# Kernel optimization log

Measured on AMD Instinct MI355X. Metric: run time of the kernel, lower is better.

The kernel has to match this reference:

```python
import jax, jax.numpy as jnp
import numpy as np

HEADS = 8
DK = 64   # key_size (defaults to size_per_head)
DV = 64   # size_per_head
RATE = 4
OUT = HEADS * DV  # 512


def extract_seq_patches(x, kernel, rate):
    # x: [b, L, d] -> [b, L, kernel, d]; strided local window gather
    b, L, d = x.shape
    k_size = kernel + (rate - 1) * (kernel - 1)
    p_right = (k_size - 1) // 2
    p_left = k_size - 1 - p_right
    xp = jnp.pad(x, ((0, 0), (p_left, p_right), (0, 0)))
    patches = [xp[:, i:i + L] for i in range(0, k_size, rate)]  # kernel slices
    return jnp.stack(patches, axis=2)


def setup_inputs() -> dict:
    key = jax.random.key(0)
    k1, k2, k3, k4 = jax.random.split(key, 4)
    s = 1.0 / np.sqrt(OUT)
    x = jax.random.normal(k1, (2, 4096, OUT), dtype=jnp.float32)
    Wq = jax.random.normal(k2, (OUT, HEADS * DK), dtype=jnp.float32) * s
    Wk = jax.random.normal(k3, (OUT, HEADS * DK), dtype=jnp.float32) * s
    Wv = jax.random.normal(k4, (OUT, HEADS * DV), dtype=jnp.float32) * s
    return {"x": x, "Wq": Wq, "Wk": Wk, "Wv": Wv}


def reference(x, Wq, Wk, Wv):
    b, L, d = x.shape
    pad = RATE - L % RATE  # torch code always pads (pad=RATE when L % RATE == 0)
    xpad = jnp.pad(x, ((0, 0), (0, pad), (0, 0)))
    nL = L + pad
    n = nL // RATE
    kernel = 2 * RATE - 1  # 1 + 2*neighbors

    qw = xpad @ Wq
    kw = xpad @ Wk
    vw = xpad @ Wv

    kwp = extract_seq_patches(kw, kernel, RATE)  # [b, nL, K, H*dk]
    vwp = extract_seq_patches(vw, kernel, RATE)  # [b, nL, K, H*dv]

    # [b, h, r, n, d]
    qw = qw.reshape(b, n, RATE, HEADS, DK).transpose(0, 3, 2, 1, 4)
    kw = kw.reshape(b, n, RATE, HEADS, DK).transpose(0, 3, 2, 1, 4)
    vw = vw.reshape(b, n, RATE, HEADS, DV).transpose(0, 3, 2, 1, 4)
    # [b, h, r, n, K, d]
    kwp = kwp.reshape(b, n, RATE, kernel, HEADS, DK).transpose(0, 4, 2, 1, 3, 5)
    vwp = vwp.reshape(b, n, RATE, kernel, HEADS, DV).transpose(0, 4, 2, 1, 3, 5)

    scale = 1.0 / np.sqrt(DK)
    a = jnp.einsum('bhrnd,bhrmd->bhrnm', qw, kw) * scale    # strided scores [b,h,r,n,n]
    ap = jnp.einsum('bhrnd,bhrnkd->bhrnk', qw, kwp) * scale  # local scores  [b,h,r,n,K]

    A = jax.nn.softmax(jnp.concatenate([a, ap], axis=-1), axis=-1)
    a, ap = A[..., :n], A[..., n:]

    o = jnp.einsum('bhrnm,bhrmd->bhrnd', a, vw) + jnp.einsum('bhrnk,bhrnkd->bhrnd', ap, vwp)
    o = o.transpose(0, 3, 2, 1, 4).reshape(b, nL, HEADS * DV)
    return o[:, :L]
```

## Files before the change

### kernel.cpp

```cpp
#include <hip/hip_runtime.h>
#include <hip/hip_bf16.h>


#define BATCH 2
#define LSEQ  4096
#define DMODEL 512
#define NH    8
#define DHEAD 64
#define NPAD  1088
#define QSCALE 0.18033688011112042f

typedef __bf16 bf16x8 __attribute__((ext_vector_type(8)));
typedef __attribute__((ext_vector_type(4))) float f32x4;
typedef __attribute__((ext_vector_type(16))) float f32x16;
typedef unsigned short u16;
typedef unsigned int u32;
typedef __attribute__((ext_vector_type(8))) u16 u16x8;
typedef __attribute__((ext_vector_type(4))) u16 u16x4;
typedef __attribute__((ext_vector_type(4))) u32 u32x4;

__device__ __forceinline__ u16 f2bf(float f) {
    u32 u = __float_as_uint(f);
    u += 0x7fffu + ((u >> 16) & 1u);
    return (u16)(u >> 16);
}

__device__ __forceinline__ u32 cvtpk(float lo, float hi) {
    u32 d;
    asm("v_cvt_pk_bf16_f32 %0, %1, %2" : "=v"(d) : "v"(lo), "v"(hi));
    return d;
}

__device__ __forceinline__ void gload16(const u16* g, u16* l) {
    __builtin_amdgcn_global_load_lds(
        (const __attribute__((address_space(1))) u32*)(const void*)g,
        (__attribute__((address_space(3))) u32*)(void*)l, 16, 0, 0);
}

__device__ __forceinline__ f32x16 zero16() {
    f32x16 v;
    #pragma unroll
    for (int i = 0; i < 16; ++i) v[i] = 0.f;
    return v;
}

__global__ __launch_bounds__(256) void prep_kernel(
    const float* __restrict__ x,
    const float* __restrict__ Wq, const float* __restrict__ Wk, const float* __restrict__ Wv,
    u16* __restrict__ xb, u16* __restrict__ Wt)
{
    const int bid = blockIdx.x, tid = threadIdx.x;
    if (bid < 2048) {
        const size_t i0 = (size_t)bid * 2048 + (size_t)tid * 8;
        float4 a = *(const float4*)(x + i0);
        float4 b = *(const float4*)(x + i0 + 4);
        u16x8 o = { f2bf(a.x), f2bf(a.y), f2bf(a.z), f2bf(a.w),
                    f2bf(b.x), f2bf(b.y), f2bf(b.z), f2bf(b.w) };
        *(u16x8*)(xb + i0) = o;
    } else {
        const int wb  = bid - 2048;
        const int mat = wb >> 6;
        const int t   = wb & 63;
        const int k0  = (t >> 3) * 64, c0 = (t & 7) * 64;
        const float* W = (mat == 0) ? Wq : (mat == 1) ? Wk : Wv;
        __shared__ u16 Ws[64][72];
        #pragma unroll
        for (int i = 0; i < 4; ++i) {
            const int chunk = i * 256 + tid;
            const int kr = chunk >> 4, c4 = (chunk & 15) * 4;
            float4 v = *(const float4*)(W + (size_t)(k0 + kr) * DMODEL + c0 + c4);
            u16x4 q = { f2bf(v.x), f2bf(v.y), f2bf(v.z), f2bf(v.w) };
            *(u16x4*)&Ws[kr][c4] = q;
        }
        __syncthreads();
        const int cc = tid >> 2, kq = (tid & 3) * 16;
        alignas(16) u16 tmp[16];
        #pragma unroll
        for (int kk = 0; kk < 16; ++kk) tmp[kk] = Ws[kq + kk][cc];
        u16* dst = Wt + (size_t)(mat * 512 + c0 + cc) * DMODEL + k0 + kq;
        *(u16x8*)dst       = *(const u16x8*)&tmp[0];
        *(u16x8*)(dst + 8) = *(const u16x8*)&tmp[8];
    }
}

__global__ __launch_bounds__(256) void gemm_kernel(
    const u16* __restrict__ xb, const u16* __restrict__ Wt,
    u16* __restrict__ Qb, u16* __restrict__ Kb, u16* __restrict__ Vb)
{
    const int bid = blockIdx.x;
    const int xcd = bid & 7;
    const int j   = bid >> 3;
    const int mt  = xcd * 8 + (j / 12);
    const int nt  = j % 12;
    const int m0 = mt * 128;
    const int n0 = nt * 128;
    const int tid = threadIdx.x;
    const int w = tid >> 6, l = tid & 63, lr = l & 15, lh = l >> 4;
    const int wr = w >> 1, wc = w & 1;

    __shared__ u16 smem[16896];
    u16* As = smem;
    u16* Bs = smem + 8192;

    f32x4 acc[4][4];
    const f32x4 fzero = {0.f, 0.f, 0.f, 0.f};
    #pragma unroll
    for (int mi = 0; mi < 4; ++mi)
        #pragma unroll
        for (int nj = 0; nj < 4; ++nj) acc[mi][nj] = fzero;

    for (int kt = 0; kt < 8; ++kt) {
        const int k0 = kt * 64;
        #pragma unroll
        for (int i = 0; i < 4; ++i) {
            const int cid = i * 256 + tid;
            const int row = cid >> 3, ch = cid & 7;
            const int sch = ch ^ (row & 7);
            u16* dstA = As + (i * 256 + w * 64) * 8;
            u16* dstB = Bs + (i * 256 + w * 64) * 8;
            gload16(xb + (size_t)(m0 + row) * DMODEL + k0 + sch * 8, dstA);
            gload16(Wt + (size_t)(n0 + row) * DMODEL + k0 + sch * 8, dstB);
        }
        __syncthreads();

        #pragma unroll
        for (int kk = 0; kk < 2; ++kk) {
            const int cs = (kk * 4 + lh) ^ (lr & 7);
            bf16x8 af[4], bfr[4];
            #pragma unroll
            for (int mi = 0; mi < 4; ++mi)
                af[mi] = *(const bf16x8*)(As + (wr * 64 + mi * 16 + lr) * 64 + cs * 8);
            #pragma unroll
            for (int nj = 0; nj < 4; ++nj)
                bfr[nj] = *(const bf16x8*)(Bs + (wc * 64 + nj * 16 + lr) * 64 + cs * 8);
            #pragma unroll
            for (int mi = 0; mi < 4; ++mi)
                #pragma unroll
                for (int nj = 0; nj < 4; ++nj)
                    acc[mi][nj] = __builtin_amdgcn_mfma_f32_16x16x32_bf16(af[mi], bfr[nj], acc[mi][nj], 0, 0, 0);
        }
        __syncthreads();
    }

    const int mat = nt >> 2;
    const int hp  = nt & 3;
    if (mat < 2) {
        u16* Ob = (mat == 0) ? Qb : Kb;
        const float osc = (mat == 0) ? QSCALE : 1.0f;
        #pragma unroll
        for (int mi = 0; mi < 4; ++mi) {
            const int gmb = m0 + wr * 64 + mi * 16 + lh * 4;
            const int b = gmb >> 12;
            #pragma unroll
            for (int rr = 0; rr < 4; ++rr) {
                const int t = (gmb + rr) & 4095;
                const int n = t >> 2, r = t & 3;
                #pragma unroll
                for (int nj = 0; nj < 4; ++nj) {
                    const int c  = wc * 64 + nj * 16 + lr;
                    const int h  = hp * 2 + (c >> 6);
                    const int dk = c & 63;
                    const size_t g = ((size_t)(b * NH + h)) * 4 + r;
                    Ob[(g * NPAD + n) * DHEAD + dk] = f2bf(acc[mi][nj][rr] * osc);
                }
            }
        }
    } else {
        #pragma unroll
        for (int mi = 0; mi < 4; ++mi) {
            const int nrel = wr * 16 + mi * 4 + lh;
            #pragma unroll
            for (int nj = 0; nj < 4; ++nj) {
                const int c = wc * 64 + nj * 16 + lr;
                #pragma unroll
                for (int rr = 0; rr < 4; ++rr)
                    smem[c * 132 + rr * 32 + nrel] = f2bf(acc[mi][nj][rr]);
            }
        }
        __syncthreads();
        const int b  = m0 >> 12;
        const int nb = (m0 & 4095) >> 2;
        #pragma unroll
        for (int e = 0; e < 2; ++e) {
            const int chunk = e * 256 + tid;
            const int c = chunk & 127, r = chunk >> 7;
            const int h  = hp * 2 + (c >> 6);
            const int dv = c & 63;
            const size_t g = ((size_t)(b * NH + h)) * 4 + r;
            u16* dst = Vb + (g * DHEAD + dv) * NPAD + nb;
            const u16* src = smem + c * 132 + r * 32;
            alignas(16) u16 tmp[32];
            #pragma unroll
            for (int q8 = 0; q8 < 8; ++q8)
                *(u16x4*)&tmp[q8 * 4] = *(const u16x4*)(src + q8 * 4);
            #pragma unroll
            for (int q16 = 0; q16 < 4; ++q16)
                *(u16x8*)(dst + q16 * 8) = *(const u16x8*)&tmp[q16 * 8];
        }
    }
}

__global__ __launch_bounds__(256) void attn_kernel(
    const u16* __restrict__ Qb, const u16* __restrict__ Kb, const u16* __restrict__ Vb,
    float* __restrict__ out)
{
    const int g  = blockIdx.x;
    const int b  = g >> 5;
    const int h  = (g >> 2) & 7;
    const int r  = g & 3;
    const int q0 = blockIdx.y * 128;
    const int tid = threadIdx.x;
    const int w  = tid >> 6;
    const int l  = tid & 63;
    const int lr = l & 31;
    const int hi = l >> 5;

    const u16* Qg  = Qb + (size_t)g * NPAD * DHEAD;
    const u16* Kg  = Kb + (size_t)g * NPAD * DHEAD;
    const u16* Vtg = Vb + (size_t)g * DHEAD * NPAD;

    __shared__ u16 KV[2][2][4096];

    const int srow = tid >> 3;
    const int ssch = (tid & 7) ^ (srow & 7);
    const u16* ksrc0 = Kg  + (size_t)srow * DHEAD + ssch * 8;
    const u16* vsrc0 = Vtg + (size_t)srow * NPAD  + ssch * 8;

    bf16x8 qa[4];
    {
        const u16* qrow = Qg + (size_t)(q0 + w * 32 + lr) * DHEAD + hi * 8;
        qa[0] = *(const bf16x8*)(qrow);
        qa[1] = *(const bf16x8*)(qrow + 16);
        qa[2] = *(const bf16x8*)(qrow + 32);
        qa[3] = *(const bf16x8*)(qrow + 48);
    }

    f32x16 o0 = zero16(), o1 = zero16();
    float Lown = 0.f;
    const int qw0 = q0 + w * 32;
    const int qg  = qw0 + lr;

    gload16(ksrc0,              &KV[0][0][w * 512]);
    gload16(ksrc0 + 32 * DHEAD, &KV[0][0][2048 + w * 512]);
    gload16(vsrc0,              &KV[0][1][w * 512]);
    gload16(vsrc0 + 32 * NPAD,  &KV[0][1][2048 + w * 512]);

    for (int mt = 0; mt < 16; ++mt) {
        const int cur = mt & 1;
        if (mt < 15) {
            const size_t ko = (size_t)(mt + 1) * 64 * DHEAD;
            const int    vo = (mt + 1) * 64;
            gload16(ksrc0 + ko,              &KV[cur ^ 1][0][w * 512]);
            gload16(ksrc0 + ko + 32 * DHEAD, &KV[cur ^ 1][0][2048 + w * 512]);
            gload16(vsrc0 + vo,              &KV[cur ^ 1][1][w * 512]);
            gload16(vsrc0 + vo + 32 * NPAD,  &KV[cur ^ 1][1][2048 + w * 512]);
            asm volatile("s_waitcnt vmcnt(4)" ::: "memory");
        } else {
            asm volatile("s_waitcnt vmcnt(0)" ::: "memory");
        }
        __builtin_amdgcn_s_barrier();

        const u16* Kbuf = KV[cur][0];
        const u16* Vbuf = KV[cur][1];

        f32x16 sA = zero16(), sB = zero16();
        __builtin_amdgcn_s_setprio(1);
        #pragma unroll
        for (int c = 0; c < 4; ++c) {
            const int slot = (c * 2 + hi) ^ (lr & 7);
            bf16x8 kbA = *(const bf16x8*)(Kbuf + (lr * 8 + slot) * 8);
            bf16x8 kbB = *(const bf16x8*)(Kbuf + ((32 + lr) * 8 + slot) * 8);
            sA = __builtin_amdgcn_mfma_f32_32x32x16_bf16(kbA, qa[c], sA, 0, 0, 0);
            sB = __builtin_amdgcn_mfma_f32_32x32x16_bf16(kbB, qa[c], sB, 0, 0, 0);
        }
        __builtin_amdgcn_s_setprio(0);

        const int m0 = mt * 64;
        const bool special = (m0 + 66 >= qw0) && (m0 <= qw0 + 34);
        if (!special) {
            #pragma unroll
            for (int reg = 0; reg < 16; ++reg) {
                sA[reg] = __builtin_amdgcn_exp2f(sA[reg]);
                sB[reg] = __builtin_amdgcn_exp2f(sB[reg]);
                Lown += sA[reg] + sB[reg];
            }
        } else {
            #pragma unroll
            for (int reg = 0; reg < 16; ++reg) {
                const int krel = (reg & 3) + 8 * (reg >> 2) + 4 * hi;
                {
                    const int dd = m0 + krel - qg;
                    float v = sA[reg];
                    if (dd >= -3 && dd <= 3) v += 1.0f;
                    sA[reg] = __builtin_amdgcn_exp2f(v);
                }
                {
                    const int dd = m0 + 32 + krel - qg;
                    float v = sB[reg];
                    if (dd >= -3 && dd <= 3) v += 1.0f;
                    sB[reg] = __builtin_amdgcn_exp2f(v);
                }
                Lown += sA[reg] + sB[reg];
            }
        }

        u32 pkA[8], pkB[8];
        #pragma unroll
        for (int r2 = 0; r2 < 8; ++r2) {
            pkA[r2] = cvtpk(sA[2 * r2], sA[2 * r2 + 1]);
            pkB[r2] = cvtpk(sB[2 * r2], sB[2 * r2 + 1]);
        }

        __builtin_amdgcn_s_setprio(1);
        #pragma unroll
        for (int c = 0; c < 4; ++c) {
            const int c1 = c & 1;
            u32 p0, p1, p2, p3;
            if (c < 2) { p0 = pkA[4*c1]; p1 = pkA[4*c1+1]; p2 = pkA[4*c1+2]; p3 = pkA[4*c1+3]; }
            else       { p0 = pkB[4*c1]; p1 = pkB[4*c1+1]; p2 = pkB[4*c1+2]; p3 = pkB[4*c1+3]; }
            const u32 own0  = hi ? p2 : p0;
            const u32 own1  = hi ? p3 : p1;
            const u32 send0 = hi ? p0 : p2;
            const u32 send1 = hi ? p1 : p3;
            const u32 recv0 = (u32)__shfl_xor((int)send0, 32);
            const u32 recv1 = (u32)__shfl_xor((int)send1, 32);
            u32x4 paw;
            paw.x = hi ? recv0 : own0;
            paw.y = hi ? recv1 : own1;
            paw.z = hi ? own0  : recv0;
            paw.w = hi ? own1  : recv1;
            const bf16x8 pa = __builtin_bit_cast(bf16x8, paw);

            const int slot = (c * 2 + hi) ^ (lr & 7);
            bf16x8 vb0 = *(const bf16x8*)(Vbuf + (lr * 8 + slot) * 8);
            bf16x8 vb1 = *(const bf16x8*)(Vbuf + ((32 + lr) * 8 + slot) * 8);
            o0 = __builtin_amdgcn_mfma_f32_32x32x16_bf16(pa, vb0, o0, 0, 0, 0);
            o1 = __builtin_amdgcn_mfma_f32_32x32x16_bf16(pa, vb1, o1, 0, 0, 0);
        }
        __builtin_amdgcn_s_setprio(0);
        __syncthreads();
    }

    const float Ltot = Lown + __shfl_xor(Lown, 32);
    const int coob = (qg < 3 ? 3 - qg : 0) + (qg > 1021 ? qg - 1021 : 0);
    const float inv = 1.0f / (Ltot + (float)(coob + 1 + (qg >= 1021 ? 1 : 0)));

    float iv[16];
    #pragma unroll
    for (int reg = 0; reg < 16; ++reg)
        iv[reg] = __shfl(inv, (reg & 3) + 8 * (reg >> 2) + 4 * hi);

    #pragma unroll
    for (int reg = 0; reg < 16; ++reg) {
        const int qrel = (reg & 3) + 8 * (reg >> 2) + 4 * hi;
        const int t = (q0 + w * 32 + qrel) * 4 + r;
        float* orow = out + ((size_t)b * LSEQ + t) * DMODEL + h * DHEAD;
        orow[lr]      = o0[reg] * iv[reg];
        orow[32 + lr] = o1[reg] * iv[reg];
    }
}

extern "C" void kernel_launch(void* const* d_in, const int* in_sizes, int n_in,
                              void* d_out, int out_size, void* d_ws, size_t ws_size,
                              hipStream_t stream) {
    const float* x  = (const float*)d_in[0];
    const float* Wq = (const float*)d_in[1];
    const float* Wk = (const float*)d_in[2];
    const float* Wv = (const float*)d_in[3];
    float* out = (float*)d_out;

    const size_t SZ = (size_t)BATCH * NH * 4 * NPAD * DHEAD;
    u16* Qb = (u16*)d_ws;
    u16* Kb = Qb + SZ;
    u16* Vb = Kb + SZ;

    u16* xb = (u16*)d_out;
    u16* Wt = xb + (size_t)8192 * 512;

    prep_kernel<<<2240, 256, 0, stream>>>(x, Wq, Wk, Wv, xb, Wt);

    gemm_kernel<<<768, 256, 0, stream>>>(xb, Wt, Qb, Kb, Vb);

    dim3 ga(64, 8);
    attn_kernel<<<ga, 256, 0, stream>>>(Qb, Kb, Vb, out);
}
```

Before: 67.68 us.

## Split attention key range across two wave groups with shared-memory reduction

Doubles the attention block to 512 threads, so two groups of four waves each process half of the key tiles (8 iterations instead of 16) for the same 128 queries. Partial output accumulators and row sums from the second group are reduced through shared memory before normalization and the store. The aim is to halve the serial loop length per block and raise waves per CU, since the grid has only 512 blocks. The cost is doubled LDS per block, an extra reduction phase with barriers, and tighter register limits from the new launch bounds.

```diff
diff --git a/kernel.cpp b/kernel.cpp
--- a/kernel.cpp
+++ b/kernel.cpp
@@ -200,7 +200,7 @@
     }
 }
 
-__global__ __launch_bounds__(256) void attn_kernel(
+__global__ __launch_bounds__(512, 4) void attn_kernel(
     const u16* __restrict__ Qb, const u16* __restrict__ Kb, const u16* __restrict__ Vb,
     float* __restrict__ out)
 {
@@ -211,6 +211,8 @@
     const int q0 = blockIdx.y * 128;
     const int tid = threadIdx.x;
     const int w  = tid >> 6;
+    const int wq = w & 3;
+    const int kh = w >> 2;
     const int l  = tid & 63;
     const int lr = l & 31;
     const int hi = l >> 5;
@@ -219,7 +221,9 @@
     const u16* Kg  = Kb + (size_t)g * NPAD * DHEAD;
     const u16* Vtg = Vb + (size_t)g * DHEAD * NPAD;
 
-    __shared__ u16 KV[2][2][4096];
+    __shared__ __align__(16) u16 KV[2][2][2][4096];
+    float* red  = (float*)&KV[0][0][0][0];
+    float* redL = red + 4 * 64 * 33;
 
     const int srow = tid >> 3;
     const int ssch = (tid & 7) ^ (srow & 7);
@@ -228,7 +232,7 @@
 
     bf16x8 qa[4];
     {
-        const u16* qrow = Qg + (size_t)(q0 + w * 32 + lr) * DHEAD + hi * 8;
+        const u16* qrow = Qg + (size_t)(q0 + wq * 32 + lr) * DHEAD + hi * 8;
         qa[0] = *(const bf16x8*)(qrow);
         qa[1] = *(const bf16x8*)(qrow + 16);
         qa[2] = *(const bf16x8*)(qrow + 32);
@@ -237,31 +241,31 @@
 
     f32x16 o0 = zero16(), o1 = zero16();
     float Lown = 0.f;
-    const int qw0 = q0 + w * 32;
+    const int qw0 = q0 + wq * 32;
     const int qg  = qw0 + lr;
 
-    gload16(ksrc0,              &KV[0][0][w * 512]);
-    gload16(ksrc0 + 32 * DHEAD, &KV[0][0][2048 + w * 512]);
-    gload16(vsrc0,              &KV[0][1][w * 512]);
-    gload16(vsrc0 + 32 * NPAD,  &KV[0][1][2048 + w * 512]);
-
-    for (int mt = 0; mt < 16; ++mt) {
+    gload16(ksrc0,                      &KV[0][0][0][w * 512]);
+    gload16(ksrc0 + (size_t)512 * DHEAD, &KV[0][1][0][w * 512]);
+    gload16(vsrc0,                      &KV[0][0][1][w * 512]);
+    gload16(vsrc0 + 512,                &KV[0][1][1][w * 512]);
+
+    for (int mt = 0; mt < 8; ++mt) {
         const int cur = mt & 1;
-        if (mt < 15) {
+        if (mt < 7) {
             const size_t ko = (size_t)(mt + 1) * 64 * DHEAD;
             const int    vo = (mt + 1) * 64;
-            gload16(ksrc0 + ko,              &KV[cur ^ 1][0][w * 512]);
-            gload16(ksrc0 + ko + 32 * DHEAD, &KV[cur ^ 1][0][2048 + w * 512]);
-            gload16(vsrc0 + vo,              &KV[cur ^ 1][1][w * 512]);
-            gload16(vsrc0 + vo + 32 * NPAD,  &KV[cur ^ 1][1][2048 + w * 512]);
+            gload16(ksrc0 + ko,                       &KV[cur ^ 1][0][0][w * 512]);
+            gload16(ksrc0 + ko + (size_t)512 * DHEAD, &KV[cur ^ 1][1][0][w * 512]);
+            gload16(vsrc0 + vo,                       &KV[cur ^ 1][0][1][w * 512]);
+            gload16(vsrc0 + vo + 512,                 &KV[cur ^ 1][1][1][w * 512]);
             asm volatile("s_waitcnt vmcnt(4)" ::: "memory");
         } else {
             asm volatile("s_waitcnt vmcnt(0)" ::: "memory");
         }
         __builtin_amdgcn_s_barrier();
 
-        const u16* Kbuf = KV[cur][0];
-        const u16* Vbuf = KV[cur][1];
+        const u16* Kbuf = &KV[cur][kh][0][0];
+        const u16* Vbuf = &KV[cur][kh][1][0];
 
         f32x16 sA = zero16(), sB = zero16();
         __builtin_amdgcn_s_setprio(1);
@@ -275,8 +279,8 @@
         }
         __builtin_amdgcn_s_setprio(0);
 
-        const int m0 = mt * 64;
-        const bool special = (m0 + 66 >= qw0) && (m0 <= qw0 + 34);
+        const int mabs = kh * 512 + mt * 64;
+        const bool special = (mabs + 66 >= qw0) && (mabs <= qw0 + 34);
         if (!special) {
             #pragma unroll
             for (int reg = 0; reg < 16; ++reg) {
@@ -289,13 +293,13 @@
             for (int reg = 0; reg < 16; ++reg) {
                 const int krel = (reg & 3) + 8 * (reg >> 2) + 4 * hi;
                 {
-                    const int dd = m0 + krel - qg;
+                    const int dd = mabs + krel - qg;
                     float v = sA[reg];
                     if (dd >= -3 && dd <= 3) v += 1.0f;
                     sA[reg] = __builtin_amdgcn_exp2f(v);
                 }
                 {
-                    const int dd = m0 + 32 + krel - qg;
+                    const int dd = mabs + 32 + krel - qg;
                     float v = sB[reg];
                     if (dd >= -3 && dd <= 3) v += 1.0f;
                     sB[reg] = __builtin_amdgcn_exp2f(v);
@@ -338,25 +342,46 @@
             o1 = __builtin_amdgcn_mfma_f32_32x32x16_bf16(pa, vb1, o1, 0, 0, 0);
         }
         __builtin_amdgcn_s_setprio(0);
-        __syncthreads();
-    }
-
-    const float Ltot = Lown + __shfl_xor(Lown, 32);
-    const int coob = (qg < 3 ? 3 - qg : 0) + (qg > 1021 ? qg - 1021 : 0);
-    const float inv = 1.0f / (Ltot + (float)(coob + 1 + (qg >= 1021 ? 1 : 0)));
-
-    float iv[16];
-    #pragma unroll
-    for (int reg = 0; reg < 16; ++reg)
-        iv[reg] = __shfl(inv, (reg & 3) + 8 * (reg >> 2) + 4 * hi);
-
-    #pragma unroll
-    for (int reg = 0; reg < 16; ++reg) {
-        const int qrel = (reg & 3) + 8 * (reg >> 2) + 4 * hi;
-        const int t = (q0 + w * 32 + qrel) * 4 + r;
-        float* orow = out + ((size_t)b * LSEQ + t) * DMODEL + h * DHEAD;
-        orow[lr]      = o0[reg] * iv[reg];
-        orow[32 + lr] = o1[reg] * iv[reg];
+        if (mt < 7) __syncthreads();
+    }
+
+    __syncthreads();
+    if (kh == 1) {
+        float* dst = red + ((size_t)wq * 64 + l) * 33;
+        #pragma unroll
+        for (int reg = 0; reg < 16; ++reg) {
+            dst[reg]      = o0[reg];
+            dst[16 + reg] = o1[reg];
+        }
+        redL[wq * 64 + l] = Lown;
+    }
+    __syncthreads();
+    if (kh == 0) {
+        const float* src = red + ((size_t)wq * 64 + l) * 33;
+        #pragma unroll
+        for (int reg = 0; reg < 16; ++reg) {
+            o0[reg] += src[reg];
+            o1[reg] += src[16 + reg];
+        }
+        Lown += redL[wq * 64 + l];
+
+        const float Ltot = Lown + __shfl_xor(Lown, 32);
+        const int coob = (qg < 3 ? 3 - qg : 0) + (qg > 1021 ? qg - 1021 : 0);
+        const float inv = 1.0f / (Ltot + (float)(coob + 1 + (qg >= 1021 ? 1 : 0)));
+
+        float iv[16];
+        #pragma unroll
+        for (int reg = 0; reg < 16; ++reg)
+            iv[reg] = __shfl(inv, (reg & 3) + 8 * (reg >> 2) + 4 * hi);
+
+        #pragma unroll
+        for (int reg = 0; reg < 16; ++reg) {
+            const int qrel = (reg & 3) + 8 * (reg >> 2) + 4 * hi;
+            const int t = (q0 + wq * 32 + qrel) * 4 + r;
+            float* orow = out + ((size_t)b * LSEQ + t) * DMODEL + h * DHEAD;
+            orow[lr]      = o0[reg] * iv[reg];
+            orow[32 + lr] = o1[reg] * iv[reg];
+        }
     }
 }
 
@@ -382,5 +407,5 @@
     gemm_kernel<<<768, 256, 0, stream>>>(xb, Wt, Qb, Kb, Vb);
 
     dim3 ga(64, 8);
-    attn_kernel<<<ga, 256, 0, stream>>>(Qb, Kb, Vb, out);
-}
+    attn_kernel<<<ga, 512, 0, stream>>>(Qb, Kb, Vb, out);
+}
```

After: 69.19 us. 2.2% more time.
